# Optimization experiments

Measured on AMD Instinct MI355X. Metric: run time of the kernel, lower is better.

## Reference

```python
import jax, jax.numpy as jnp
import numpy as np
import math

D = 128
LAMBDA_INIT = 0.8 - 0.6 * math.exp(-0.3 * 1)  # depth=1


def _clin(xr, xi, wr, wi, br, bi):
    # complex linear: (xr + i xi) @ (wr + i wi)^T + (br + i bi)
    o_r = jnp.einsum('bhsd,od->bhso', xr, wr) - jnp.einsum('bhsd,od->bhso', xi, wi) + br
    o_i = jnp.einsum('bhsd,od->bhso', xr, wi) + jnp.einsum('bhsd,od->bhso', xi, wr) + bi
    return o_r, o_i


def setup_inputs() -> dict:
    key = jax.random.key(0)
    ks = jax.random.split(key, 32)
    B, H, S = 1, 12, 1024
    shp = (B, H, S, D)
    inp = {}
    names = ['q_r', 'q_i', 'k_r', 'k_i', 'v_r', 'v_i', 'pe_q_r', 'pe_q_i', 'pe_k_r', 'pe_k_i']
    for i, n in enumerate(names):
        inp[n] = jax.random.normal(ks[i], shp, dtype=jnp.float32)
    std = 1.0 / math.sqrt(D)
    inp['qw_r'] = jax.random.normal(ks[10], (2 * D, D), jnp.float32) * std
    inp['qw_i'] = jax.random.normal(ks[11], (2 * D, D), jnp.float32) * std
    inp['qb_r'] = jnp.zeros((2 * D,), jnp.float32)
    inp['qb_i'] = jnp.zeros((2 * D,), jnp.float32)
    for j, p in enumerate(['k', 'v', 'g', 'o']):
        inp[p + 'w_r'] = jax.random.normal(ks[12 + 2 * j], (D, D), jnp.float32) * std
        inp[p + 'w_i'] = jax.random.normal(ks[13 + 2 * j], (D, D), jnp.float32) * std
        inp[p + 'b_r'] = jnp.zeros((D,), jnp.float32)
        inp[p + 'b_i'] = jnp.zeros((D,), jnp.float32)
    inp['lq1'] = jax.random.normal(ks[20], (D,), jnp.float32) * 0.1
    inp['lk1'] = jax.random.normal(ks[21], (D,), jnp.float32) * 0.1
    inp['lq2'] = jax.random.normal(ks[22], (D,), jnp.float32) * 0.1
    inp['lk2'] = jax.random.normal(ks[23], (D,), jnp.float32) * 0.1
    inp['sub_w'] = jnp.ones((2 * D,), jnp.float32)
    return inp


def _forward(q_r, q_i, k_r, k_i, v_r, v_i, pe_q_r, pe_q_i, pe_k_r, pe_k_i,
             qw_r, qw_i, qb_r, qb_i, kw_r, kw_i, kb_r, kb_i,
             vw_r, vw_i, vb_r, vb_i, gw_r, gw_i, gb_r, gb_i,
             ow_r, ow_i, ob_r, ob_i, lq1, lk1, lq2, lk2, sub_w):
    scale = D ** (-0.5)
    qp_r, qp_i = _clin(q_r, q_i, qw_r, qw_i, qb_r, qb_i)   # [B,H,S,2D]
    kp_r, kp_i = _clin(k_r, k_i, kw_r, kw_i, kb_r, kb_i)   # [B,H,S,D]
    vp_r, vp_i = _clin(v_r, v_i, vw_r, vw_i, vb_r, vb_i)
    qp_r = qp_r + jnp.concatenate([pe_q_r, pe_q_r], axis=-1)
    qp_i = qp_i + jnp.concatenate([pe_q_i, pe_q_i], axis=-1)
    kp_r = kp_r + pe_k_r
    kp_i = kp_i + pe_k_i
    q1_r, q2_r = jnp.split(qp_r, 2, axis=-1)
    q1_i, q2_i = jnp.split(qp_i, 2, axis=-1)

    def attn_w(qr, qi):
        s_r = jnp.einsum('bhqd,bhkd->bhqk', qr, kp_r) + jnp.einsum('bhqd,bhkd->bhqk', qi, kp_i)
        s_i = jnp.einsum('bhqd,bhkd->bhqk', qi, kp_r) - jnp.einsum('bhqd,bhkd->bhqk', qr, kp_i)
        mag = jnp.sqrt(s_r ** 2 + s_i ** 2 + 1e-8) * scale
        return jax.nn.softmax(mag.astype(jnp.float32), axis=-1).astype(s_r.dtype)

    w1 = attn_w(q1_r, q1_i)
    w2 = attn_w(q2_r, q2_i)
    a1_r = jnp.einsum('bhqk,bhkd->bhqd', w1, vp_r)
    a1_i = jnp.einsum('bhqk,bhkd->bhqd', w1, vp_i)
    a2_r = jnp.einsum('bhqk,bhkd->bhqd', w2, vp_r)
    a2_i = jnp.einsum('bhqk,bhkd->bhqd', w2, vp_i)
    cat_r = jnp.concatenate([a1_r, a2_r], axis=-1)
    cat_i = jnp.concatenate([a1_i, a2_i], axis=-1)
    rms = jnp.sqrt(jnp.mean(cat_r ** 2 + cat_i ** 2, axis=-1, keepdims=True) + 1e-5)
    cat_r = cat_r / rms * sub_w
    cat_i = cat_i / rms * sub_w
    a1_r, a2_r = jnp.split(cat_r, 2, axis=-1)
    a1_i, a2_i = jnp.split(cat_i, 2, axis=-1)
    lam1 = jnp.exp(jnp.sum(lq1 * lk1))
    lam2 = jnp.exp(jnp.sum(lq2 * lk2))
    lam = jax.nn.sigmoid(lam1 - lam2 + LAMBDA_INIT)
    out_r = a1_r - lam * a2_r
    out_i = a1_i - lam * a2_i
    g_r, g_i = _clin(q_r, q_i, gw_r, gw_i, gb_r, gb_i)
    out_r, out_i = g_r * out_r - g_i * out_i, g_r * out_i + g_i * out_r
    out_r, out_i = _clin(out_r, out_i, ow_r, ow_i, ob_r, ob_i)
    return out_r, out_i


def reference(q_r, q_i, k_r, k_i, v_r, v_i, pe_q_r, pe_q_i, pe_k_r, pe_k_i,
              qw_r, qw_i, qb_r, qb_i, kw_r, kw_i, kb_r, kb_i,
              vw_r, vw_i, vb_r, vb_i, gw_r, gw_i, gb_r, gb_i,
              ow_r, ow_i, ob_r, ob_i, lq1, lk1, lq2, lk2, sub_w):
    return _forward(q_r, q_i, k_r, k_i, v_r, v_i, pe_q_r, pe_q_i, pe_k_r, pe_k_i,
                    qw_r, qw_i, qb_r, qb_i, kw_r, kw_i, kb_r, kb_i,
                    vw_r, vw_i, vb_r, vb_i, gw_r, gw_i, gb_r, gb_i,
                    ow_r, ow_i, ob_r, ob_i, lq1, lk1, lq2, lk2, sub_w)
```

## Files before the change

### kernel.cpp

```cpp
#include <hip/hip_runtime.h>
#include <math.h>

#define H 12
#define S 1024
#define D 128
#define NROWS (H * S)

typedef __attribute__((ext_vector_type(8))) _Float16 f16x8;
typedef __attribute__((ext_vector_type(4))) float f32x4;
typedef __attribute__((ext_vector_type(4))) int i32x4;

__device__ __forceinline__ short f2h(float f) {
    _Float16 h = (_Float16)f;
    return __builtin_bit_cast(short, h);
}
__device__ __forceinline__ float h2f(short s) {
    return (float)__builtin_bit_cast(_Float16, s);
}
__device__ __forceinline__ f16x8 fneg8(f16x8 v) {
    i32x4 u = __builtin_bit_cast(i32x4, v);
    u ^= (int)0x80008000;
    return __builtin_bit_cast(f16x8, u);
}

#define WS_QP_R   0ULL
#define WS_QP_I   6291456ULL
#define WS_KP_R   12582912ULL
#define WS_KP_I   15728640ULL
#define WS_VPT_R  18874368ULL
#define WS_VPT_I  22020096ULL
#define WS_GP_R   25165824ULL
#define WS_GP_I   28311552ULL
#define WS_ACAT_R 31457280ULL
#define WS_ACAT_I 37748736ULL
#define WS_LAM    44040192ULL
#define WS_SC     44040448ULL
#define W16_PER_HEAD   4194304ULL
#define STAT_PER_HEAD  16384ULL

__global__ void lam_kernel(const float* __restrict__ lq1, const float* __restrict__ lk1,
                           const float* __restrict__ lq2, const float* __restrict__ lk2,
                           float* __restrict__ lam_out)
{
    int t = threadIdx.x;
    float p1 = lq1[t] * lk1[t];
    float p2 = lq2[t] * lk2[t];
    #pragma unroll
    for (int off = 32; off; off >>= 1) {
        p1 += __shfl_xor(p1, off);
        p2 += __shfl_xor(p2, off);
    }
    __shared__ float s1[2], s2[2];
    if ((t & 63) == 0) { s1[t >> 6] = p1; s2[t >> 6] = p2; }
    __syncthreads();
    if (t == 0) {
        float l1 = expf(s1[0] + s1[1]);
        float l2 = expf(s2[0] + s2[1]);
        float x = l1 - l2 + 0.3555090675909693f;
        lam_out[0] = 1.0f / (1.0f + expf(-x));
    }
}

__global__ __launch_bounds__(256) void proj_all(
    const float* __restrict__ q_r, const float* __restrict__ q_i,
    const float* __restrict__ k_r, const float* __restrict__ k_i,
    const float* __restrict__ v_r, const float* __restrict__ v_i,
    const float* __restrict__ pe_q_r, const float* __restrict__ pe_q_i,
    const float* __restrict__ pe_k_r, const float* __restrict__ pe_k_i,
    const float* __restrict__ qw_r, const float* __restrict__ qw_i,
    const float* __restrict__ qb_r, const float* __restrict__ qb_i,
    const float* __restrict__ kw_r, const float* __restrict__ kw_i,
    const float* __restrict__ kb_r, const float* __restrict__ kb_i,
    const float* __restrict__ vw_r, const float* __restrict__ vw_i,
    const float* __restrict__ vb_r, const float* __restrict__ vb_i,
    const float* __restrict__ gw_r, const float* __restrict__ gw_i,
    const float* __restrict__ gb_r, const float* __restrict__ gb_i,
    short* __restrict__ qp_r, short* __restrict__ qp_i,
    short* __restrict__ kp_r, short* __restrict__ kp_i,
    short* __restrict__ vpT_r, short* __restrict__ vpT_i,
    short* __restrict__ gp_r, short* __restrict__ gp_i)
{
    const int y = blockIdx.y;
    const float *xr, *xi, *wr, *wi, *br, *bi, *per = nullptr, *pei = nullptr;
    short *outr_, *outi_;
    int M, omode, col0;
    if (y < 4)      { xr = q_r; xi = q_i; wr = qw_r; wi = qw_i; br = qb_r; bi = qb_i;
                      per = pe_q_r; pei = pe_q_i; outr_ = qp_r; outi_ = qp_i;
                      M = 256; omode = 1; col0 = y * 64; }
    else if (y < 6) { xr = k_r; xi = k_i; wr = kw_r; wi = kw_i; br = kb_r; bi = kb_i;
                      per = pe_k_r; pei = pe_k_i; outr_ = kp_r; outi_ = kp_i;
                      M = 128; omode = 1; col0 = (y - 4) * 64; }
    else if (y < 8) { xr = v_r; xi = v_i; wr = vw_r; wi = vw_i; br = vb_r; bi = vb_i;
                      outr_ = vpT_r; outi_ = vpT_i;
                      M = 128; omode = 2; col0 = (y - 6) * 64; }
    else            { xr = q_r; xi = q_i; wr = gw_r; wi = gw_i; br = gb_r; bi = gb_i;
                      outr_ = gp_r; outi_ = gp_i;
                      M = 128; omode = 1; col0 = (y - 8) * 64; }

    __shared__ short As[64 * 72], Brs[64 * 72], Bis[64 * 72];
    const int t = threadIdx.x;
    const int row0 = blockIdx.x * 64;
    const int lane = t & 63, wid = t >> 6;
    const int wm = (wid >> 1) * 32, wn = (wid & 1) * 32;
    const int fm = lane & 15, fq = lane >> 4;
    f32x4 zero4 = {0.f, 0.f, 0.f, 0.f};
    f32x4 accr[2][2], acci[2][2];
    #pragma unroll
    for (int i = 0; i < 2; ++i)
        #pragma unroll
        for (int j = 0; j < 2; ++j) { accr[i][j] = zero4; acci[i][j] = zero4; }

    for (int c = 0; c < 4; ++c) {
        const bool hi = (c >= 2);
        const int kb = (c & 1) * 64;
        const float* Asrc = hi ? xi : xr;
        const float* Brsrc = hi ? wi : wr;
        const float* Bisrc = hi ? wr : wi;
        const float bsign = hi ? -1.0f : 1.0f;
        __syncthreads();
        #pragma unroll
        for (int it = 0; it < 4; ++it) {
            int lin = it * 256 + t;
            int r = lin >> 4, k4 = (lin & 15) * 4;
            float4 va = *(const float4*)&Asrc[(size_t)(row0 + r) * 128 + kb + k4];
            *(short4*)&As[r * 72 + k4] = make_short4(f2h(va.x), f2h(va.y), f2h(va.z), f2h(va.w));
            float4 vr = *(const float4*)&Brsrc[(size_t)(col0 + r) * 128 + kb + k4];
            *(short4*)&Brs[r * 72 + k4] = make_short4(f2h(bsign * vr.x), f2h(bsign * vr.y),
                                                      f2h(bsign * vr.z), f2h(bsign * vr.w));
            float4 vi = *(const float4*)&Bisrc[(size_t)(col0 + r) * 128 + kb + k4];
            *(short4*)&Bis[r * 72 + k4] = make_short4(f2h(vi.x), f2h(vi.y), f2h(vi.z), f2h(vi.w));
        }
        __syncthreads();
        #pragma unroll
        for (int ks = 0; ks < 64; ks += 32) {
            f16x8 bfr[2], bfi[2];
            #pragma unroll
            for (int j = 0; j < 2; ++j) {
                bfr[j] = *(const f16x8*)&Brs[(wn + j * 16 + fm) * 72 + ks + fq * 8];
                bfi[j] = *(const f16x8*)&Bis[(wn + j * 16 + fm) * 72 + ks + fq * 8];
            }
            #pragma unroll
            for (int i = 0; i < 2; ++i) {
                f16x8 a = *(const f16x8*)&As[(wm + i * 16 + fm) * 72 + ks + fq * 8];
                #pragma unroll
                for (int j = 0; j < 2; ++j) {
                    accr[i][j] = __builtin_amdgcn_mfma_f32_16x16x32_f16(a, bfr[j], accr[i][j], 0, 0, 0);
                    acci[i][j] = __builtin_amdgcn_mfma_f32_16x16x32_f16(a, bfi[j], acci[i][j], 0, 0, 0);
                }
            }
        }
    }
    #pragma unroll
    for (int i = 0; i < 2; ++i)
        #pragma unroll
        for (int j = 0; j < 2; ++j) {
            int colc = col0 + wn + j * 16 + fm;
            float bbr = br[colc], bbi = bi[colc];
            if (omode == 2) {
                int rb = row0 + wm + i * 16 + fq * 4;
                int hq = rb >> 10, sq = rb & 1023;
                short4 o_r4 = make_short4(f2h(accr[i][j][0] + bbr), f2h(accr[i][j][1] + bbr),
                                          f2h(accr[i][j][2] + bbr), f2h(accr[i][j][3] + bbr));
                short4 o_i4 = make_short4(f2h(acci[i][j][0] + bbi), f2h(acci[i][j][1] + bbi),
                                          f2h(acci[i][j][2] + bbi), f2h(acci[i][j][3] + bbi));
                size_t ob = ((size_t)(hq * 128 + colc)) * 1024 + sq;
                *(short4*)&outr_[ob] = o_r4;
                *(short4*)&outi_[ob] = o_i4;
            } else {
                #pragma unroll
                for (int reg = 0; reg < 4; ++reg) {
                    int rr = row0 + wm + i * 16 + fq * 4 + reg;
                    float o_r = accr[i][j][reg] + bbr;
                    float o_i = acci[i][j][reg] + bbi;
                    if (per) {
                        o_r += per[(size_t)rr * 128 + (colc & 127)];
                        o_i += pei[(size_t)rr * 128 + (colc & 127)];
                    }
                    outr_[(size_t)rr * M + colc] = f2h(o_r);
                    outi_[(size_t)rr * M + colc] = f2h(o_i);
                }
            }
        }
}

__global__ __launch_bounds__(256) void oproj_mfma(
    const short* __restrict__ gp_r, const short* __restrict__ gp_i,
    const float* __restrict__ wr, const float* __restrict__ wi,
    const float* __restrict__ br, const float* __restrict__ bi,
    float* __restrict__ outr, float* __restrict__ outi)
{
    __shared__ short As[64 * 72], Brs[64 * 72], Bis[64 * 72];
    const int t = threadIdx.x;
    const int row0 = blockIdx.x * 64, col0 = blockIdx.y * 64;
    const int lane = t & 63, wid = t >> 6;
    const int wm = (wid >> 1) * 32, wn = (wid & 1) * 32;
    const int fm = lane & 15, fq = lane >> 4;
    f32x4 zero4 = {0.f, 0.f, 0.f, 0.f};
    f32x4 accr[2][2], acci[2][2];
    #pragma unroll
    for (int i = 0; i < 2; ++i)
        #pragma unroll
        for (int j = 0; j < 2; ++j) { accr[i][j] = zero4; acci[i][j] = zero4; }

    for (int c = 0; c < 4; ++c) {
        const bool hi = (c >= 2);
        const int kb = (c & 1) * 64;
        const short* Asrc = hi ? gp_i : gp_r;
        const float* Brsrc = hi ? wi : wr;
        const float* Bisrc = hi ? wr : wi;
        const float bsign = hi ? -1.0f : 1.0f;
        __syncthreads();
        #pragma unroll
        for (int it = 0; it < 4; ++it) {
            int lin = it * 256 + t;
            int r = lin >> 4, k4 = (lin & 15) * 4;
            *(short4*)&As[r * 72 + k4] = *(const short4*)&Asrc[(size_t)(row0 + r) * 128 + kb + k4];
            float4 vr = *(const float4*)&Brsrc[(size_t)(col0 + r) * 128 + kb + k4];
            *(short4*)&Brs[r * 72 + k4] = make_short4(f2h(bsign * vr.x), f2h(bsign * vr.y),
                                                      f2h(bsign * vr.z), f2h(bsign * vr.w));
            float4 vi = *(const float4*)&Bisrc[(size_t)(col0 + r) * 128 + kb + k4];
            *(short4*)&Bis[r * 72 + k4] = make_short4(f2h(vi.x), f2h(vi.y), f2h(vi.z), f2h(vi.w));
        }
        __syncthreads();
        #pragma unroll
        for (int ks = 0; ks < 64; ks += 32) {
            f16x8 bfr[2], bfi[2];
            #pragma unroll
            for (int j = 0; j < 2; ++j) {
                bfr[j] = *(const f16x8*)&Brs[(wn + j * 16 + fm) * 72 + ks + fq * 8];
                bfi[j] = *(const f16x8*)&Bis[(wn + j * 16 + fm) * 72 + ks + fq * 8];
            }
            #pragma unroll
            for (int i = 0; i < 2; ++i) {
                f16x8 a = *(const f16x8*)&As[(wm + i * 16 + fm) * 72 + ks + fq * 8];
                #pragma unroll
                for (int j = 0; j < 2; ++j) {
                    accr[i][j] = __builtin_amdgcn_mfma_f32_16x16x32_f16(a, bfr[j], accr[i][j], 0, 0, 0);
                    acci[i][j] = __builtin_amdgcn_mfma_f32_16x16x32_f16(a, bfi[j], acci[i][j], 0, 0, 0);
                }
            }
        }
    }
    #pragma unroll
    for (int i = 0; i < 2; ++i)
        #pragma unroll
        for (int j = 0; j < 2; ++j) {
            int colc = col0 + wn + j * 16 + fm;
            float bbr = br[colc], bbi = bi[colc];
            #pragma unroll
            for (int reg = 0; reg < 4; ++reg) {
                int rr = row0 + wm + i * 16 + fq * 4 + reg;
                outr[(size_t)rr * 128 + colc] = accr[i][j][reg] + bbr;
                outi[(size_t)rr * 128 + colc] = acci[i][j][reg] + bbi;
            }
        }
}

__global__ __launch_bounds__(256) void score_mfma(
    const short* __restrict__ qp_r, const short* __restrict__ qp_i,
    const short* __restrict__ kp_r, const short* __restrict__ kp_i,
    short* __restrict__ w16, int h0)
{
    __shared__ short Qr[64 * 72], Qi[64 * 72], Kt[128 * 72];
    const int t = threadIdx.x;
    const int hh = blockIdx.z >> 1, map = blockIdx.z & 1;
    const int h = h0 + hh;
    const int q0 = blockIdx.x * 64, c0 = blockIdx.y * 128;
    const int lane = t & 63, wid = t >> 6;
    const int wm = (wid >> 1) * 32, wn = (wid & 1) * 64;
    const int fm = lane & 15, fq = lane >> 4;
    f32x4 zero4 = {0.f, 0.f, 0.f, 0.f};
    f32x4 sr[2][4], si[2][4];
    #pragma unroll
    for (int i = 0; i < 2; ++i)
        #pragma unroll
        for (int j = 0; j < 4; ++j) { sr[i][j] = zero4; si[i][j] = zero4; }

    for (int kb = 0; kb < 2; ++kb) {
        const int kbase = map * 128 + kb * 64;
        __syncthreads();
        #pragma unroll
        for (int i = 0; i < 4; ++i) {
            int lin = i * 256 + t;
            int r = lin >> 4, k4 = (lin & 15) * 4;
            size_t qb = (size_t)(h * S + q0 + r) * 256 + kbase + k4;
            *(short4*)&Qr[r * 72 + k4] = *(const short4*)&qp_r[qb];
            *(short4*)&Qi[r * 72 + k4] = *(const short4*)&qp_i[qb];
        }
        #pragma unroll
        for (int i = 0; i < 8; ++i) {
            int lin = i * 256 + t;
            int r = lin >> 4, k4 = (lin & 15) * 4;
            *(short4*)&Kt[r * 72 + k4] =
                *(const short4*)&kp_r[(size_t)(h * S + c0 + r) * 128 + kb * 64 + k4];
        }
        __syncthreads();
        f16x8 aR[2][2], aI[2][2];
        #pragma unroll
        for (int ks = 0; ks < 2; ++ks)
            #pragma unroll
            for (int i = 0; i < 2; ++i) {
                int ao = (wm + i * 16 + fm) * 72 + ks * 32 + fq * 8;
                aR[ks][i] = *(const f16x8*)&Qr[ao];
                aI[ks][i] = *(const f16x8*)&Qi[ao];
            }
        #pragma unroll
        for (int ks = 0; ks < 2; ++ks) {
            f16x8 b[4];
            #pragma unroll
            for (int j = 0; j < 4; ++j)
                b[j] = *(const f16x8*)&Kt[(wn + j * 16 + fm) * 72 + ks * 32 + fq * 8];
            #pragma unroll
            for (int i = 0; i < 2; ++i)
                #pragma unroll
                for (int j = 0; j < 4; ++j) {
                    sr[i][j] = __builtin_amdgcn_mfma_f32_16x16x32_f16(aR[ks][i], b[j], sr[i][j], 0, 0, 0);
                    si[i][j] = __builtin_amdgcn_mfma_f32_16x16x32_f16(aI[ks][i], b[j], si[i][j], 0, 0, 0);
                }
        }
        __syncthreads();
        #pragma unroll
        for (int i = 0; i < 8; ++i) {
            int lin = i * 256 + t;
            int r = lin >> 4, k4 = (lin & 15) * 4;
            *(short4*)&Kt[r * 72 + k4] =
                *(const short4*)&kp_i[(size_t)(h * S + c0 + r) * 128 + kb * 64 + k4];
        }
        __syncthreads();
        #pragma unroll
        for (int ks = 0; ks < 2; ++ks) {
            f16x8 b[4];
            #pragma unroll
            for (int j = 0; j < 4; ++j)
                b[j] = *(const f16x8*)&Kt[(wn + j * 16 + fm) * 72 + ks * 32 + fq * 8];
            f16x8 nR0 = fneg8(aR[ks][0]), nR1 = fneg8(aR[ks][1]);
            #pragma unroll
            for (int j = 0; j < 4; ++j) {
                sr[0][j] = __builtin_amdgcn_mfma_f32_16x16x32_f16(aI[ks][0], b[j], sr[0][j], 0, 0, 0);
                si[0][j] = __builtin_amdgcn_mfma_f32_16x16x32_f16(nR0, b[j], si[0][j], 0, 0, 0);
                sr[1][j] = __builtin_amdgcn_mfma_f32_16x16x32_f16(aI[ks][1], b[j], sr[1][j], 0, 0, 0);
                si[1][j] = __builtin_amdgcn_mfma_f32_16x16x32_f16(nR1, b[j], si[1][j], 0, 0, 0);
            }
        }
    }
    const float scale = 0.08838834764831845f;
    #pragma unroll
    for (int i = 0; i < 2; ++i)
        #pragma unroll
        for (int j = 0; j < 4; ++j) {
            int kcol = c0 + wn + j * 16 + fm;
            #pragma unroll
            for (int reg = 0; reg < 4; ++reg) {
                int q = q0 + wm + i * 16 + fq * 4 + reg;
                float r1 = sr[i][j][reg], I1 = si[i][j][reg];
                float m1 = sqrtf(fmaf(r1, r1, fmaf(I1, I1, 1e-8f))) * scale;
                w16[(((size_t)hh * 2 + map) * S + q) * S + kcol] = f2h(m1);
            }
        }
}

__global__ __launch_bounds__(256) void smstats(const short* __restrict__ w16,
                                               float2* __restrict__ stats)
{
    const short* row = w16 + (size_t)blockIdx.x * S;
    int t = threadIdx.x;
    short4 s = ((const short4*)row)[t];
    float f0 = h2f(s.x), f1 = h2f(s.y), f2v = h2f(s.z), f3 = h2f(s.w);
    float m = fmaxf(fmaxf(f0, f1), fmaxf(f2v, f3));
    #pragma unroll
    for (int off = 32; off; off >>= 1) m = fmaxf(m, __shfl_xor(m, off));
    __shared__ float redm[4], reds[4];
    int w = t >> 6;
    if ((t & 63) == 0) redm[w] = m;
    __syncthreads();
    m = fmaxf(fmaxf(redm[0], redm[1]), fmaxf(redm[2], redm[3]));
    float ssum = __expf(f0 - m) + __expf(f1 - m) + __expf(f2v - m) + __expf(f3 - m);
    #pragma unroll
    for (int off = 32; off; off >>= 1) ssum += __shfl_xor(ssum, off);
    if ((t & 63) == 0) reds[w] = ssum;
    __syncthreads();
    if (t == 0) {
        float total = reds[0] + reds[1] + reds[2] + reds[3];
        stats[blockIdx.x] = make_float2(m, 1.0f / total);
    }
}

__global__ __launch_bounds__(256) void av_mfma(
    const short* __restrict__ w16, const float2* __restrict__ stats,
    const short* __restrict__ vpT_r, const short* __restrict__ vpT_i,
    short* __restrict__ acat_r, short* __restrict__ acat_i, int h0)
{
    __shared__ short W1[32 * 72], W2[32 * 72], Vc[128 * 72];
    const int t = threadIdx.x;
    const int hh = blockIdx.z, h = h0 + hh;
    const int comp = blockIdx.y;
    const int q0 = blockIdx.x * 32;
    const short* vpT = comp ? vpT_i : vpT_r;
    short* acat = comp ? acat_i : acat_r;
    const float2* st1 = stats + ((size_t)hh * 2 + 0) * S;
    const float2* st2 = stats + ((size_t)hh * 2 + 1) * S;
    const int lane = t & 63, wid = t >> 6;
    const int wm = (wid >> 1) * 16, wn = (wid & 1) * 64;
    const int fm = lane & 15, fq = lane >> 4;
    f32x4 zero4 = {0.f, 0.f, 0.f, 0.f};
    f32x4 a1[4], a2[4];
    #pragma unroll
    for (int j = 0; j < 4; ++j) { a1[j] = zero4; a2[j] = zero4; }

    for (int k0 = 0; k0 < S; k0 += 64) {
        __syncthreads();
        #pragma unroll
        for (int it = 0; it < 2; ++it) {
            int lin = it * 256 + t;
            int r = lin >> 4, k4 = (lin & 15) * 4;
            float2 s1v = st1[q0 + r];
            float2 s2v = st2[q0 + r];
            short4 m1 = *(const short4*)&w16[(((size_t)hh * 2 + 0) * S + q0 + r) * S + k0 + k4];
            short4 m2 = *(const short4*)&w16[(((size_t)hh * 2 + 1) * S + q0 + r) * S + k0 + k4];
            *(short4*)&W1[r * 72 + k4] = make_short4(
                f2h(__expf(h2f(m1.x) - s1v.x) * s1v.y), f2h(__expf(h2f(m1.y) - s1v.x) * s1v.y),
                f2h(__expf(h2f(m1.z) - s1v.x) * s1v.y), f2h(__expf(h2f(m1.w) - s1v.x) * s1v.y));
            *(short4*)&W2[r * 72 + k4] = make_short4(
                f2h(__expf(h2f(m2.x) - s2v.x) * s2v.y), f2h(__expf(h2f(m2.y) - s2v.x) * s2v.y),
                f2h(__expf(h2f(m2.z) - s2v.x) * s2v.y), f2h(__expf(h2f(m2.w) - s2v.x) * s2v.y));
        }
        #pragma unroll
        for (int it = 0; it < 8; ++it) {
            int lin = it * 256 + t;
            int dd = lin >> 4, k4 = (lin & 15) * 4;
            *(short4*)&Vc[dd * 72 + k4] = *(const short4*)&vpT[(size_t)(h * 128 + dd) * 1024 + k0 + k4];
        }
        __syncthreads();
        #pragma unroll
        for (int ks = 0; ks < 64; ks += 32) {
            f16x8 b[4];
            #pragma unroll
            for (int j = 0; j < 4; ++j)
                b[j] = *(const f16x8*)&Vc[(wn + j * 16 + fm) * 72 + ks + fq * 8];
            int wo = (wm + fm) * 72 + ks + fq * 8;
            f16x8 w1f = *(const f16x8*)&W1[wo];
            f16x8 w2f = *(const f16x8*)&W2[wo];
            #pragma unroll
            for (int j = 0; j < 4; ++j) {
                a1[j] = __builtin_amdgcn_mfma_f32_16x16x32_f16(w1f, b[j], a1[j], 0, 0, 0);
                a2[j] = __builtin_amdgcn_mfma_f32_16x16x32_f16(w2f, b[j], a2[j], 0, 0, 0);
            }
        }
    }
    #pragma unroll
    for (int j = 0; j < 4; ++j) {
        int d = wn + j * 16 + fm;
        #pragma unroll
        for (int reg = 0; reg < 4; ++reg) {
            int q = q0 + wm + fq * 4 + reg;
            size_t rowb = (size_t)(h * S + q) * 256;
            acat[rowb + d]       = f2h(a1[j][reg]);
            acat[rowb + 128 + d] = f2h(a2[j][reg]);
        }
    }
}

__global__ __launch_bounds__(256) void rmsgate_kernel(
    const short* __restrict__ acat_r, const short* __restrict__ acat_i,
    const float* __restrict__ sub_w, const float* __restrict__ lam_ptr,
    short* __restrict__ gp_r, short* __restrict__ gp_i)
{
    int row = blockIdx.x;
    int t = threadIdx.x;
    float ar = h2f(acat_r[(size_t)row * 256 + t]);
    float ai = h2f(acat_i[(size_t)row * 256 + t]);
    float ss = fmaf(ar, ar, ai * ai);
    #pragma unroll
    for (int off = 32; off; off >>= 1) ss += __shfl_xor(ss, off);
    __shared__ float red[4];
    if ((t & 63) == 0) red[t >> 6] = ss;
    __syncthreads();
    float total = red[0] + red[1] + red[2] + red[3];
    float inv_rms = 1.0f / sqrtf(total * (1.0f / 256.0f) + 1e-5f);
    float sw = sub_w[t];
    __shared__ float Cr[256], Ci[256];
    Cr[t] = ar * inv_rms * sw;
    Ci[t] = ai * inv_rms * sw;
    __syncthreads();
    if (t < 128) {
        float lam = lam_ptr[0];
        float o_r = Cr[t] - lam * Cr[t + 128];
        float o_i = Ci[t] - lam * Ci[t + 128];
        float gr = h2f(gp_r[(size_t)row * 128 + t]);
        float gi = h2f(gp_i[(size_t)row * 128 + t]);
        gp_r[(size_t)row * 128 + t] = f2h(gr * o_r - gi * o_i);
        gp_i[(size_t)row * 128 + t] = f2h(gr * o_i + gi * o_r);
    }
}

extern "C" void kernel_launch(void* const* d_in, const int* in_sizes, int n_in,
                              void* d_out, int out_size, void* d_ws, size_t ws_size,
                              hipStream_t stream)
{
    (void)in_sizes; (void)n_in; (void)out_size;
    const float* q_r    = (const float*)d_in[0];
    const float* q_i    = (const float*)d_in[1];
    const float* k_r    = (const float*)d_in[2];
    const float* k_i    = (const float*)d_in[3];
    const float* v_r    = (const float*)d_in[4];
    const float* v_i    = (const float*)d_in[5];
    const float* pe_q_r = (const float*)d_in[6];
    const float* pe_q_i = (const float*)d_in[7];
    const float* pe_k_r = (const float*)d_in[8];
    const float* pe_k_i = (const float*)d_in[9];
    const float* qw_r   = (const float*)d_in[10];
    const float* qw_i   = (const float*)d_in[11];
    const float* qb_r   = (const float*)d_in[12];
    const float* qb_i   = (const float*)d_in[13];
    const float* kw_r   = (const float*)d_in[14];
    const float* kw_i   = (const float*)d_in[15];
    const float* kb_r   = (const float*)d_in[16];
    const float* kb_i   = (const float*)d_in[17];
    const float* vw_r   = (const float*)d_in[18];
    const float* vw_i   = (const float*)d_in[19];
    const float* vb_r   = (const float*)d_in[20];
    const float* vb_i   = (const float*)d_in[21];
    const float* gw_r   = (const float*)d_in[22];
    const float* gw_i   = (const float*)d_in[23];
    const float* gb_r   = (const float*)d_in[24];
    const float* gb_i   = (const float*)d_in[25];
    const float* ow_r   = (const float*)d_in[26];
    const float* ow_i   = (const float*)d_in[27];
    const float* ob_r   = (const float*)d_in[28];
    const float* ob_i   = (const float*)d_in[29];
    const float* lq1    = (const float*)d_in[30];
    const float* lk1    = (const float*)d_in[31];
    const float* lq2    = (const float*)d_in[32];
    const float* lk2    = (const float*)d_in[33];
    const float* sub_w  = (const float*)d_in[34];

    char* ws = (char*)d_ws;
    short* qp_r   = (short*)(ws + WS_QP_R);
    short* qp_i   = (short*)(ws + WS_QP_I);
    short* kp_r   = (short*)(ws + WS_KP_R);
    short* kp_i   = (short*)(ws + WS_KP_I);
    short* vpT_r  = (short*)(ws + WS_VPT_R);
    short* vpT_i  = (short*)(ws + WS_VPT_I);
    short* gp_r   = (short*)(ws + WS_GP_R);
    short* gp_i   = (short*)(ws + WS_GP_I);
    short* acat_r = (short*)(ws + WS_ACAT_R);
    short* acat_i = (short*)(ws + WS_ACAT_I);
    float* lam    = (float*)(ws + WS_LAM);
    short* w16    = (short*)(ws + WS_SC);

    float* out_r = (float*)d_out;
    float* out_i = out_r + (size_t)NROWS * D;

    size_t avail = ws_size > WS_SC ? ws_size - WS_SC : 0;
    int nh_chunk = (int)(avail / (W16_PER_HEAD + STAT_PER_HEAD));
    if (nh_chunk < 1) nh_chunk = 1;
    if (nh_chunk > H) nh_chunk = H;
    float2* stats = (float2*)(ws + WS_SC + (size_t)nh_chunk * W16_PER_HEAD);

    lam_kernel<<<1, 128, 0, stream>>>(lq1, lk1, lq2, lk2, lam);

    proj_all<<<dim3(192, 10), 256, 0, stream>>>(
        q_r, q_i, k_r, k_i, v_r, v_i, pe_q_r, pe_q_i, pe_k_r, pe_k_i,
        qw_r, qw_i, qb_r, qb_i, kw_r, kw_i, kb_r, kb_i,
        vw_r, vw_i, vb_r, vb_i, gw_r, gw_i, gb_r, gb_i,
        qp_r, qp_i, kp_r, kp_i, vpT_r, vpT_i, gp_r, gp_i);

    for (int h0 = 0; h0 < H; h0 += nh_chunk) {
        int nhh = (H - h0 < nh_chunk) ? (H - h0) : nh_chunk;
        score_mfma<<<dim3(16, 8, nhh * 2), 256, 0, stream>>>(qp_r, qp_i, kp_r, kp_i, w16, h0);
        smstats<<<nhh * 2 * S, 256, 0, stream>>>(w16, stats);
        av_mfma<<<dim3(32, 2, nhh), 256, 0, stream>>>(w16, stats, vpT_r, vpT_i, acat_r, acat_i, h0);
    }

    rmsgate_kernel<<<NROWS, 256, 0, stream>>>(acat_r, acat_i, sub_w, lam, gp_r, gp_i);

    oproj_mfma<<<dim3(192, 2), 256, 0, stream>>>(gp_r, gp_i, ow_r, ow_i, ob_r, ob_i, out_r, out_i);
}
```

Measured before the change: 296.7 us.

## Fuse all stages into one cooperative persistent kernel with grid syncs

Turns projection, score, softmax stats, AV, RMS-gate and output projection into device functions run by a single persistent cooperative kernel, with grid-wide barriers between stages, and keeps the multi-launch path as a fallback. The aim is to remove the per-launch overhead and tail idle time of about seven separate kernel launches. In exchange, grid.sync barriers add their own cost and work is spread over a fixed grid (up to 2048 blocks), so per-stage load balance and occupancy may get worse. The cooperative path only runs when the workspace is large enough to hold all heads at once.

```diff
diff --git a/kernel.cpp b/kernel.cpp
--- a/kernel.cpp
+++ b/kernel.cpp
@@ -1,5 +1,8 @@
 #include <hip/hip_runtime.h>
+#include <hip/hip_cooperative_groups.h>
 #include <math.h>
+
+namespace cg = cooperative_groups;
 
 #define H 12
 #define S 1024
@@ -37,69 +40,47 @@
 #define WS_SC     44040448ULL
 #define W16_PER_HEAD   4194304ULL
 #define STAT_PER_HEAD  16384ULL
-
-__global__ void lam_kernel(const float* __restrict__ lq1, const float* __restrict__ lk1,
-                           const float* __restrict__ lq2, const float* __restrict__ lk2,
-                           float* __restrict__ lam_out)
-{
-    int t = threadIdx.x;
-    float p1 = lq1[t] * lk1[t];
-    float p2 = lq2[t] * lk2[t];
-    #pragma unroll
-    for (int off = 32; off; off >>= 1) {
-        p1 += __shfl_xor(p1, off);
-        p2 += __shfl_xor(p2, off);
-    }
-    __shared__ float s1[2], s2[2];
-    if ((t & 63) == 0) { s1[t >> 6] = p1; s2[t >> 6] = p2; }
-    __syncthreads();
-    if (t == 0) {
-        float l1 = expf(s1[0] + s1[1]);
-        float l2 = expf(s2[0] + s2[1]);
-        float x = l1 - l2 + 0.3555090675909693f;
-        lam_out[0] = 1.0f / (1.0f + expf(-x));
-    }
-}
-
-__global__ __launch_bounds__(256) void proj_all(
-    const float* __restrict__ q_r, const float* __restrict__ q_i,
-    const float* __restrict__ k_r, const float* __restrict__ k_i,
-    const float* __restrict__ v_r, const float* __restrict__ v_i,
-    const float* __restrict__ pe_q_r, const float* __restrict__ pe_q_i,
-    const float* __restrict__ pe_k_r, const float* __restrict__ pe_k_i,
-    const float* __restrict__ qw_r, const float* __restrict__ qw_i,
-    const float* __restrict__ qb_r, const float* __restrict__ qb_i,
-    const float* __restrict__ kw_r, const float* __restrict__ kw_i,
-    const float* __restrict__ kb_r, const float* __restrict__ kb_i,
-    const float* __restrict__ vw_r, const float* __restrict__ vw_i,
-    const float* __restrict__ vb_r, const float* __restrict__ vb_i,
-    const float* __restrict__ gw_r, const float* __restrict__ gw_i,
-    const float* __restrict__ gb_r, const float* __restrict__ gb_i,
-    short* __restrict__ qp_r, short* __restrict__ qp_i,
-    short* __restrict__ kp_r, short* __restrict__ kp_i,
-    short* __restrict__ vpT_r, short* __restrict__ vpT_i,
-    short* __restrict__ gp_r, short* __restrict__ gp_i)
-{
-    const int y = blockIdx.y;
+#define WS_STATS_FULL  (WS_SC + 12ULL * W16_PER_HEAD)
+#define WS_NEED_FULL   (WS_STATS_FULL + 24576ULL * 8ULL)
+
+struct MegaParams {
+    const float *q_r, *q_i, *k_r, *k_i, *v_r, *v_i;
+    const float *pe_q_r, *pe_q_i, *pe_k_r, *pe_k_i;
+    const float *qw_r, *qw_i, *qb_r, *qb_i;
+    const float *kw_r, *kw_i, *kb_r, *kb_i;
+    const float *vw_r, *vw_i, *vb_r, *vb_i;
+    const float *gw_r, *gw_i, *gb_r, *gb_i;
+    const float *ow_r, *ow_i, *ob_r, *ob_i;
+    const float *lq1, *lk1, *lq2, *lk2, *sub_w;
+    short *qp_r, *qp_i, *kp_r, *kp_i, *vpT_r, *vpT_i, *gp_r, *gp_i;
+    short *acat_r, *acat_i;
+    short *w16;
+    float *lam;
+    float2 *stats;
+    float *out_r, *out_i;
+};
+
+__device__ __forceinline__ void dev_proj(int bxx, int y, short* As, short* Brs, short* Bis,
+                                         const MegaParams& P)
+{
     const float *xr, *xi, *wr, *wi, *br, *bi, *per = nullptr, *pei = nullptr;
     short *outr_, *outi_;
     int M, omode, col0;
-    if (y < 4)      { xr = q_r; xi = q_i; wr = qw_r; wi = qw_i; br = qb_r; bi = qb_i;
-                      per = pe_q_r; pei = pe_q_i; outr_ = qp_r; outi_ = qp_i;
+    if (y < 4)      { xr = P.q_r; xi = P.q_i; wr = P.qw_r; wi = P.qw_i; br = P.qb_r; bi = P.qb_i;
+                      per = P.pe_q_r; pei = P.pe_q_i; outr_ = P.qp_r; outi_ = P.qp_i;
                       M = 256; omode = 1; col0 = y * 64; }
-    else if (y < 6) { xr = k_r; xi = k_i; wr = kw_r; wi = kw_i; br = kb_r; bi = kb_i;
-                      per = pe_k_r; pei = pe_k_i; outr_ = kp_r; outi_ = kp_i;
+    else if (y < 6) { xr = P.k_r; xi = P.k_i; wr = P.kw_r; wi = P.kw_i; br = P.kb_r; bi = P.kb_i;
+                      per = P.pe_k_r; pei = P.pe_k_i; outr_ = P.kp_r; outi_ = P.kp_i;
                       M = 128; omode = 1; col0 = (y - 4) * 64; }
-    else if (y < 8) { xr = v_r; xi = v_i; wr = vw_r; wi = vw_i; br = vb_r; bi = vb_i;
-                      outr_ = vpT_r; outi_ = vpT_i;
+    else if (y < 8) { xr = P.v_r; xi = P.v_i; wr = P.vw_r; wi = P.vw_i; br = P.vb_r; bi = P.vb_i;
+                      outr_ = P.vpT_r; outi_ = P.vpT_i;
                       M = 128; omode = 2; col0 = (y - 6) * 64; }
-    else            { xr = q_r; xi = q_i; wr = gw_r; wi = gw_i; br = gb_r; bi = gb_i;
-                      outr_ = gp_r; outi_ = gp_i;
+    else            { xr = P.q_r; xi = P.q_i; wr = P.gw_r; wi = P.gw_i; br = P.gb_r; bi = P.gb_i;
+                      outr_ = P.gp_r; outi_ = P.gp_i;
                       M = 128; omode = 1; col0 = (y - 8) * 64; }
 
-    __shared__ short As[64 * 72], Brs[64 * 72], Bis[64 * 72];
     const int t = threadIdx.x;
-    const int row0 = blockIdx.x * 64;
+    const int row0 = bxx * 64;
     const int lane = t & 63, wid = t >> 6;
     const int wm = (wid >> 1) * 32, wn = (wid & 1) * 32;
     const int fm = lane & 15, fq = lane >> 4;
@@ -183,15 +164,182 @@
         }
 }
 
-__global__ __launch_bounds__(256) void oproj_mfma(
-    const short* __restrict__ gp_r, const short* __restrict__ gp_i,
-    const float* __restrict__ wr, const float* __restrict__ wi,
-    const float* __restrict__ br, const float* __restrict__ bi,
-    float* __restrict__ outr, float* __restrict__ outi)
-{
-    __shared__ short As[64 * 72], Brs[64 * 72], Bis[64 * 72];
+__device__ __forceinline__ void dev_score(int bxx, int byy, int hhL, int map, int h,
+                                          short* Qr, short* Qi, short* Kt,
+                                          const MegaParams& P, short* w16)
+{
     const int t = threadIdx.x;
-    const int row0 = blockIdx.x * 64, col0 = blockIdx.y * 64;
+    const int q0 = bxx * 64, c0 = byy * 128;
+    const int lane = t & 63, wid = t >> 6;
+    const int wm = (wid >> 1) * 32, wn = (wid & 1) * 64;
+    const int fm = lane & 15, fq = lane >> 4;
+    f32x4 zero4 = {0.f, 0.f, 0.f, 0.f};
+    f32x4 sr[2][4], si[2][4];
+    #pragma unroll
+    for (int i = 0; i < 2; ++i)
+        #pragma unroll
+        for (int j = 0; j < 4; ++j) { sr[i][j] = zero4; si[i][j] = zero4; }
+
+    for (int kb = 0; kb < 2; ++kb) {
+        const int kbase = map * 128 + kb * 64;
+        __syncthreads();
+        #pragma unroll
+        for (int i = 0; i < 4; ++i) {
+            int lin = i * 256 + t;
+            int r = lin >> 4, k4 = (lin & 15) * 4;
+            size_t qb = (size_t)(h * S + q0 + r) * 256 + kbase + k4;
+            *(short4*)&Qr[r * 72 + k4] = *(const short4*)&P.qp_r[qb];
+            *(short4*)&Qi[r * 72 + k4] = *(const short4*)&P.qp_i[qb];
+        }
+        #pragma unroll
+        for (int i = 0; i < 8; ++i) {
+            int lin = i * 256 + t;
+            int r = lin >> 4, k4 = (lin & 15) * 4;
+            *(short4*)&Kt[r * 72 + k4] =
+                *(const short4*)&P.kp_r[(size_t)(h * S + c0 + r) * 128 + kb * 64 + k4];
+        }
+        __syncthreads();
+        f16x8 aR[2][2], aI[2][2];
+        #pragma unroll
+        for (int ks = 0; ks < 2; ++ks)
+            #pragma unroll
+            for (int i = 0; i < 2; ++i) {
+                int ao = (wm + i * 16 + fm) * 72 + ks * 32 + fq * 8;
+                aR[ks][i] = *(const f16x8*)&Qr[ao];
+                aI[ks][i] = *(const f16x8*)&Qi[ao];
+            }
+        #pragma unroll
+        for (int ks = 0; ks < 2; ++ks) {
+            f16x8 b[4];
+            #pragma unroll
+            for (int j = 0; j < 4; ++j)
+                b[j] = *(const f16x8*)&Kt[(wn + j * 16 + fm) * 72 + ks * 32 + fq * 8];
+            #pragma unroll
+            for (int i = 0; i < 2; ++i)
+                #pragma unroll
+                for (int j = 0; j < 4; ++j) {
+                    sr[i][j] = __builtin_amdgcn_mfma_f32_16x16x32_f16(aR[ks][i], b[j], sr[i][j], 0, 0, 0);
+                    si[i][j] = __builtin_amdgcn_mfma_f32_16x16x32_f16(aI[ks][i], b[j], si[i][j], 0, 0, 0);
+                }
+        }
+        __syncthreads();
+        #pragma unroll
+        for (int i = 0; i < 8; ++i) {
+            int lin = i * 256 + t;
+            int r = lin >> 4, k4 = (lin & 15) * 4;
+            *(short4*)&Kt[r * 72 + k4] =
+                *(const short4*)&P.kp_i[(size_t)(h * S + c0 + r) * 128 + kb * 64 + k4];
+        }
+        __syncthreads();
+        #pragma unroll
+        for (int ks = 0; ks < 2; ++ks) {
+            f16x8 b[4];
+            #pragma unroll
+            for (int j = 0; j < 4; ++j)
+                b[j] = *(const f16x8*)&Kt[(wn + j * 16 + fm) * 72 + ks * 32 + fq * 8];
+            f16x8 nR0 = fneg8(aR[ks][0]), nR1 = fneg8(aR[ks][1]);
+            #pragma unroll
+            for (int j = 0; j < 4; ++j) {
+                sr[0][j] = __builtin_amdgcn_mfma_f32_16x16x32_f16(aI[ks][0], b[j], sr[0][j], 0, 0, 0);
+                si[0][j] = __builtin_amdgcn_mfma_f32_16x16x32_f16(nR0, b[j], si[0][j], 0, 0, 0);
+                sr[1][j] = __builtin_amdgcn_mfma_f32_16x16x32_f16(aI[ks][1], b[j], sr[1][j], 0, 0, 0);
+                si[1][j] = __builtin_amdgcn_mfma_f32_16x16x32_f16(nR1, b[j], si[1][j], 0, 0, 0);
+            }
+        }
+    }
+    const float scale = 0.08838834764831845f;
+    #pragma unroll
+    for (int i = 0; i < 2; ++i)
+        #pragma unroll
+        for (int j = 0; j < 4; ++j) {
+            int kcol = c0 + wn + j * 16 + fm;
+            #pragma unroll
+            for (int reg = 0; reg < 4; ++reg) {
+                int q = q0 + wm + i * 16 + fq * 4 + reg;
+                float r1 = sr[i][j][reg], I1 = si[i][j][reg];
+                float m1 = sqrtf(fmaf(r1, r1, fmaf(I1, I1, 1e-8f))) * scale;
+                w16[(((size_t)hhL * 2 + map) * S + q) * S + kcol] = f2h(m1);
+            }
+        }
+}
+
+__device__ __forceinline__ void dev_av(int bxx, int comp, int hhL, int h,
+                                       short* W1, short* W2, short* Vc,
+                                       const MegaParams& P, const short* w16,
+                                       const float2* stats)
+{
+    const int t = threadIdx.x;
+    const int q0 = bxx * 32;
+    const short* vpT = comp ? P.vpT_i : P.vpT_r;
+    short* acat = comp ? P.acat_i : P.acat_r;
+    const float2* st1 = stats + ((size_t)hhL * 2 + 0) * S;
+    const float2* st2 = stats + ((size_t)hhL * 2 + 1) * S;
+    const int lane = t & 63, wid = t >> 6;
+    const int wm = (wid >> 1) * 16, wn = (wid & 1) * 64;
+    const int fm = lane & 15, fq = lane >> 4;
+    f32x4 zero4 = {0.f, 0.f, 0.f, 0.f};
+    f32x4 a1[4], a2[4];
+    #pragma unroll
+    for (int j = 0; j < 4; ++j) { a1[j] = zero4; a2[j] = zero4; }
+
+    for (int k0 = 0; k0 < S; k0 += 64) {
+        __syncthreads();
+        #pragma unroll
+        for (int it = 0; it < 2; ++it) {
+            int lin = it * 256 + t;
+            int r = lin >> 4, k4 = (lin & 15) * 4;
+            float2 s1v = st1[q0 + r];
+            float2 s2v = st2[q0 + r];
+            short4 m1 = *(const short4*)&w16[(((size_t)hhL * 2 + 0) * S + q0 + r) * S + k0 + k4];
+            short4 m2 = *(const short4*)&w16[(((size_t)hhL * 2 + 1) * S + q0 + r) * S + k0 + k4];
+            *(short4*)&W1[r * 72 + k4] = make_short4(
+                f2h(__expf(h2f(m1.x) - s1v.x) * s1v.y), f2h(__expf(h2f(m1.y) - s1v.x) * s1v.y),
+                f2h(__expf(h2f(m1.z) - s1v.x) * s1v.y), f2h(__expf(h2f(m1.w) - s1v.x) * s1v.y));
+            *(short4*)&W2[r * 72 + k4] = make_short4(
+                f2h(__expf(h2f(m2.x) - s2v.x) * s2v.y), f2h(__expf(h2f(m2.y) - s2v.x) * s2v.y),
+                f2h(__expf(h2f(m2.z) - s2v.x) * s2v.y), f2h(__expf(h2f(m2.w) - s2v.x) * s2v.y));
+        }
+        #pragma unroll
+        for (int it = 0; it < 8; ++it) {
+            int lin = it * 256 + t;
+            int dd = lin >> 4, k4 = (lin & 15) * 4;
+            *(short4*)&Vc[dd * 72 + k4] = *(const short4*)&vpT[(size_t)(h * 128 + dd) * 1024 + k0 + k4];
+        }
+        __syncthreads();
+        #pragma unroll
+        for (int ks = 0; ks < 64; ks += 32) {
+            f16x8 b[4];
+            #pragma unroll
+            for (int j = 0; j < 4; ++j)
+                b[j] = *(const f16x8*)&Vc[(wn + j * 16 + fm) * 72 + ks + fq * 8];
+            int wo = (wm + fm) * 72 + ks + fq * 8;
+            f16x8 w1f = *(const f16x8*)&W1[wo];
+            f16x8 w2f = *(const f16x8*)&W2[wo];
+            #pragma unroll
+            for (int j = 0; j < 4; ++j) {
+                a1[j] = __builtin_amdgcn_mfma_f32_16x16x32_f16(w1f, b[j], a1[j], 0, 0, 0);
+                a2[j] = __builtin_amdgcn_mfma_f32_16x16x32_f16(w2f, b[j], a2[j], 0, 0, 0);
+            }
+        }
+    }
+    #pragma unroll
+    for (int j = 0; j < 4; ++j) {
+        int d = wn + j * 16 + fm;
+        #pragma unroll
+        for (int reg = 0; reg < 4; ++reg) {
+            int q = q0 + wm + fq * 4 + reg;
+            size_t rowb = (size_t)(h * S + q) * 256;
+            acat[rowb + d]       = f2h(a1[j][reg]);
+            acat[rowb + 128 + d] = f2h(a2[j][reg]);
+        }
+    }
+}
+
+__device__ __forceinline__ void dev_oproj(int bxx, int byy, short* As, short* Brs, short* Bis,
+                                          const MegaParams& P)
+{
+    const int t = threadIdx.x;
+    const int row0 = bxx * 64, col0 = byy * 64;
     const int lane = t & 63, wid = t >> 6;
     const int wm = (wid >> 1) * 32, wn = (wid & 1) * 32;
     const int fm = lane & 15, fq = lane >> 4;
@@ -205,9 +353,9 @@
     for (int c = 0; c < 4; ++c) {
         const bool hi = (c >= 2);
         const int kb = (c & 1) * 64;
-        const short* Asrc = hi ? gp_i : gp_r;
-        const float* Brsrc = hi ? wi : wr;
-        const float* Bisrc = hi ? wr : wi;
+        const short* Asrc = hi ? P.gp_i : P.gp_r;
+        const float* Brsrc = hi ? P.ow_i : P.ow_r;
+        const float* Bisrc = hi ? P.ow_r : P.ow_i;
         const float bsign = hi ? -1.0f : 1.0f;
         __syncthreads();
         #pragma unroll
@@ -246,123 +394,188 @@
         #pragma unroll
         for (int j = 0; j < 2; ++j) {
             int colc = col0 + wn + j * 16 + fm;
-            float bbr = br[colc], bbi = bi[colc];
+            float bbr = P.ob_r[colc], bbi = P.ob_i[colc];
             #pragma unroll
             for (int reg = 0; reg < 4; ++reg) {
                 int rr = row0 + wm + i * 16 + fq * 4 + reg;
-                outr[(size_t)rr * 128 + colc] = accr[i][j][reg] + bbr;
-                outi[(size_t)rr * 128 + colc] = acci[i][j][reg] + bbi;
-            }
-        }
-}
-
-__global__ __launch_bounds__(256) void score_mfma(
-    const short* __restrict__ qp_r, const short* __restrict__ qp_i,
-    const short* __restrict__ kp_r, const short* __restrict__ kp_i,
-    short* __restrict__ w16, int h0)
-{
-    __shared__ short Qr[64 * 72], Qi[64 * 72], Kt[128 * 72];
-    const int t = threadIdx.x;
-    const int hh = blockIdx.z >> 1, map = blockIdx.z & 1;
-    const int h = h0 + hh;
-    const int q0 = blockIdx.x * 64, c0 = blockIdx.y * 128;
-    const int lane = t & 63, wid = t >> 6;
-    const int wm = (wid >> 1) * 32, wn = (wid & 1) * 64;
-    const int fm = lane & 15, fq = lane >> 4;
-    f32x4 zero4 = {0.f, 0.f, 0.f, 0.f};
-    f32x4 sr[2][4], si[2][4];
-    #pragma unroll
-    for (int i = 0; i < 2; ++i)
-        #pragma unroll
-        for (int j = 0; j < 4; ++j) { sr[i][j] = zero4; si[i][j] = zero4; }
-
-    for (int kb = 0; kb < 2; ++kb) {
-        const int kbase = map * 128 + kb * 64;
-        __syncthreads();
-        #pragma unroll
-        for (int i = 0; i < 4; ++i) {
-            int lin = i * 256 + t;
-            int r = lin >> 4, k4 = (lin & 15) * 4;
-            size_t qb = (size_t)(h * S + q0 + r) * 256 + kbase + k4;
-            *(short4*)&Qr[r * 72 + k4] = *(const short4*)&qp_r[qb];
-            *(short4*)&Qi[r * 72 + k4] = *(const short4*)&qp_i[qb];
-        }
-        #pragma unroll
-        for (int i = 0; i < 8; ++i) {
-            int lin = i * 256 + t;
-            int r = lin >> 4, k4 = (lin & 15) * 4;
-            *(short4*)&Kt[r * 72 + k4] =
-                *(const short4*)&kp_r[(size_t)(h * S + c0 + r) * 128 + kb * 64 + k4];
-        }
-        __syncthreads();
-        f16x8 aR[2][2], aI[2][2];
-        #pragma unroll
-        for (int ks = 0; ks < 2; ++ks)
-            #pragma unroll
-            for (int i = 0; i < 2; ++i) {
-                int ao = (wm + i * 16 + fm) * 72 + ks * 32 + fq * 8;
-                aR[ks][i] = *(const f16x8*)&Qr[ao];
-                aI[ks][i] = *(const f16x8*)&Qi[ao];
-            }
-        #pragma unroll
-        for (int ks = 0; ks < 2; ++ks) {
-            f16x8 b[4];
-            #pragma unroll
-            for (int j = 0; j < 4; ++j)
-                b[j] = *(const f16x8*)&Kt[(wn + j * 16 + fm) * 72 + ks * 32 + fq * 8];
-            #pragma unroll
-            for (int i = 0; i < 2; ++i)
+                P.out_r[(size_t)rr * 128 + colc] = accr[i][j][reg] + bbr;
+                P.out_i[(size_t)rr * 128 + colc] = acci[i][j][reg] + bbi;
+            }
+        }
+}
+
+__global__ __launch_bounds__(256) void mega(MegaParams P)
+{
+    cg::grid_group gg = cg::this_grid();
+    __shared__ __align__(16) char SM[36864];
+    const int nb = (int)gridDim.x, bid = (int)blockIdx.x;
+    const int t = threadIdx.x, lane = t & 63, wid = t >> 6;
+
+    {
+        float p1 = (t < 128) ? P.lq1[t] * P.lk1[t] : 0.f;
+        float p2 = (t < 128) ? P.lq2[t] * P.lk2[t] : 0.f;
+        #pragma unroll
+        for (int off = 32; off; off >>= 1) {
+            p1 += __shfl_xor(p1, off);
+            p2 += __shfl_xor(p2, off);
+        }
+        float* s1 = (float*)SM;
+        float* s2 = s1 + 4;
+        if ((t & 63) == 0) { s1[wid] = p1; s2[wid] = p2; }
+        __syncthreads();
+        if (bid == 0 && t == 0) {
+            float l1 = expf(s1[0] + s1[1] + s1[2] + s1[3]);
+            float l2 = expf(s2[0] + s2[1] + s2[2] + s2[3]);
+            float x = l1 - l2 + 0.3555090675909693f;
+            P.lam[0] = 1.0f / (1.0f + expf(-x));
+        }
+        __syncthreads();
+    }
+
+    {
+        short* As = (short*)SM;
+        short* Brs = As + 64 * 72;
+        short* Bis = Brs + 64 * 72;
+        for (int it = bid; it < 1920; it += nb)
+            dev_proj(it % 192, it / 192, As, Brs, Bis, P);
+    }
+    gg.sync();
+
+    {
+        short* Qr = (short*)SM;
+        short* Qi = Qr + 64 * 72;
+        short* Kt = Qi + 64 * 72;
+        for (int it = bid; it < 3072; it += nb) {
+            int z = it / 128;
+            dev_score(it % 16, (it / 16) % 8, z >> 1, z & 1, z >> 1, Qr, Qi, Kt, P, P.w16);
+        }
+    }
+    gg.sync();
+
+    for (int row = bid * 4 + wid; row < 2 * NROWS; row += nb * 4) {
+        const short* rp = P.w16 + (size_t)row * S;
+        short4 v0 = ((const short4*)rp)[lane];
+        short4 v1 = ((const short4*)rp)[lane + 64];
+        short4 v2 = ((const short4*)rp)[lane + 128];
+        short4 v3 = ((const short4*)rp)[lane + 192];
+        float f[16] = {h2f(v0.x), h2f(v0.y), h2f(v0.z), h2f(v0.w),
+                       h2f(v1.x), h2f(v1.y), h2f(v1.z), h2f(v1.w),
+                       h2f(v2.x), h2f(v2.y), h2f(v2.z), h2f(v2.w),
+                       h2f(v3.x), h2f(v3.y), h2f(v3.z), h2f(v3.w)};
+        float m = f[0];
+        #pragma unroll
+        for (int j = 1; j < 16; ++j) m = fmaxf(m, f[j]);
+        #pragma unroll
+        for (int off = 32; off; off >>= 1) m = fmaxf(m, __shfl_xor(m, off));
+        float ssum = 0.f;
+        #pragma unroll
+        for (int j = 0; j < 16; ++j) ssum += __expf(f[j] - m);
+        #pragma unroll
+        for (int off = 32; off; off >>= 1) ssum += __shfl_xor(ssum, off);
+        if (lane == 0) P.stats[row] = make_float2(m, 1.0f / ssum);
+    }
+    gg.sync();
+
+    {
+        short* W1 = (short*)SM;
+        short* W2 = W1 + 32 * 72;
+        short* Vc = W2 + 32 * 72;
+        for (int it = bid; it < 768; it += nb)
+            dev_av(it % 32, (it / 32) % 2, it / 64, it / 64, W1, W2, Vc, P, P.w16, P.stats);
+    }
+    gg.sync();
+
+    {
+        const float lam = P.lam[0];
+        for (int row = bid * 4 + wid; row < NROWS; row += nb * 4) {
+            short4 ar4 = ((const short4*)(P.acat_r + (size_t)row * 256))[lane];
+            short4 ai4 = ((const short4*)(P.acat_i + (size_t)row * 256))[lane];
+            float ar[4] = {h2f(ar4.x), h2f(ar4.y), h2f(ar4.z), h2f(ar4.w)};
+            float ai[4] = {h2f(ai4.x), h2f(ai4.y), h2f(ai4.z), h2f(ai4.w)};
+            float ss = 0.f;
+            #pragma unroll
+            for (int j = 0; j < 4; ++j) ss = fmaf(ar[j], ar[j], fmaf(ai[j], ai[j], ss));
+            #pragma unroll
+            for (int off = 32; off; off >>= 1) ss += __shfl_xor(ss, off);
+            float inv_rms = 1.0f / sqrtf(ss * (1.0f / 256.0f) + 1e-5f);
+            float4 sw = ((const float4*)P.sub_w)[lane];
+            float Cr[4], Ci[4];
+            Cr[0] = ar[0] * inv_rms * sw.x; Ci[0] = ai[0] * inv_rms * sw.x;
+            Cr[1] = ar[1] * inv_rms * sw.y; Ci[1] = ai[1] * inv_rms * sw.y;
+            Cr[2] = ar[2] * inv_rms * sw.z; Ci[2] = ai[2] * inv_rms * sw.z;
+            Cr[3] = ar[3] * inv_rms * sw.w; Ci[3] = ai[3] * inv_rms * sw.w;
+            float pr[4], pi[4];
+            #pragma unroll
+            for (int j = 0; j < 4; ++j) {
+                pr[j] = __shfl_xor(Cr[j], 32);
+                pi[j] = __shfl_xor(Ci[j], 32);
+            }
+            if (lane < 32) {
+                short4 gr4 = ((const short4*)(P.gp_r + (size_t)row * 128))[lane];
+                short4 gi4 = ((const short4*)(P.gp_i + (size_t)row * 128))[lane];
+                float grv[4] = {h2f(gr4.x), h2f(gr4.y), h2f(gr4.z), h2f(gr4.w)};
+                float giv[4] = {h2f(gi4.x), h2f(gi4.y), h2f(gi4.z), h2f(gi4.w)};
+                short orx[4], oix[4];
                 #pragma unroll
                 for (int j = 0; j < 4; ++j) {
-                    sr[i][j] = __builtin_amdgcn_mfma_f32_16x16x32_f16(aR[ks][i], b[j], sr[i][j], 0, 0, 0);
-                    si[i][j] = __builtin_amdgcn_mfma_f32_16x16x32_f16(aI[ks][i], b[j], si[i][j], 0, 0, 0);
+                    float o_r = Cr[j] - lam * pr[j];
+                    float o_i = Ci[j] - lam * pi[j];
+                    orx[j] = f2h(grv[j] * o_r - giv[j] * o_i);
+                    oix[j] = f2h(grv[j] * o_i + giv[j] * o_r);
                 }
-        }
-        __syncthreads();
-        #pragma unroll
-        for (int i = 0; i < 8; ++i) {
-            int lin = i * 256 + t;
-            int r = lin >> 4, k4 = (lin & 15) * 4;
-            *(short4*)&Kt[r * 72 + k4] =
-                *(const short4*)&kp_i[(size_t)(h * S + c0 + r) * 128 + kb * 64 + k4];
-        }
-        __syncthreads();
-        #pragma unroll
-        for (int ks = 0; ks < 2; ++ks) {
-            f16x8 b[4];
-            #pragma unroll
-            for (int j = 0; j < 4; ++j)
-                b[j] = *(const f16x8*)&Kt[(wn + j * 16 + fm) * 72 + ks * 32 + fq * 8];
-            f16x8 nR0 = fneg8(aR[ks][0]), nR1 = fneg8(aR[ks][1]);
-            #pragma unroll
-            for (int j = 0; j < 4; ++j) {
-                sr[0][j] = __builtin_amdgcn_mfma_f32_16x16x32_f16(aI[ks][0], b[j], sr[0][j], 0, 0, 0);
-                si[0][j] = __builtin_amdgcn_mfma_f32_16x16x32_f16(nR0, b[j], si[0][j], 0, 0, 0);
-                sr[1][j] = __builtin_amdgcn_mfma_f32_16x16x32_f16(aI[ks][1], b[j], sr[1][j], 0, 0, 0);
-                si[1][j] = __builtin_amdgcn_mfma_f32_16x16x32_f16(nR1, b[j], si[1][j], 0, 0, 0);
-            }
-        }
-    }
-    const float scale = 0.08838834764831845f;
-    #pragma unroll
-    for (int i = 0; i < 2; ++i)
-        #pragma unroll
-        for (int j = 0; j < 4; ++j) {
-            int kcol = c0 + wn + j * 16 + fm;
-            #pragma unroll
-            for (int reg = 0; reg < 4; ++reg) {
-                int q = q0 + wm + i * 16 + fq * 4 + reg;
-                float r1 = sr[i][j][reg], I1 = si[i][j][reg];
-                float m1 = sqrtf(fmaf(r1, r1, fmaf(I1, I1, 1e-8f))) * scale;
-                w16[(((size_t)hh * 2 + map) * S + q) * S + kcol] = f2h(m1);
-            }
-        }
-}
-
-__global__ __launch_bounds__(256) void smstats(const short* __restrict__ w16,
-                                               float2* __restrict__ stats)
-{
-    const short* row = w16 + (size_t)blockIdx.x * S;
+                ((short4*)(P.gp_r + (size_t)row * 128))[lane] = make_short4(orx[0], orx[1], orx[2], orx[3]);
+                ((short4*)(P.gp_i + (size_t)row * 128))[lane] = make_short4(oix[0], oix[1], oix[2], oix[3]);
+            }
+        }
+    }
+    gg.sync();
+
+    {
+        short* As = (short*)SM;
+        short* Brs = As + 64 * 72;
+        short* Bis = Brs + 64 * 72;
+        for (int it = bid; it < 384; it += nb)
+            dev_oproj(it % 192, it / 192, As, Brs, Bis, P);
+    }
+}
+
+__global__ void lam_k(MegaParams P)
+{
+    int t = threadIdx.x;
+    float p1 = P.lq1[t] * P.lk1[t];
+    float p2 = P.lq2[t] * P.lk2[t];
+    #pragma unroll
+    for (int off = 32; off; off >>= 1) {
+        p1 += __shfl_xor(p1, off);
+        p2 += __shfl_xor(p2, off);
+    }
+    __shared__ float s1[2], s2[2];
+    if ((t & 63) == 0) { s1[t >> 6] = p1; s2[t >> 6] = p2; }
+    __syncthreads();
+    if (t == 0) {
+        float l1 = expf(s1[0] + s1[1]);
+        float l2 = expf(s2[0] + s2[1]);
+        float x = l1 - l2 + 0.3555090675909693f;
+        P.lam[0] = 1.0f / (1.0f + expf(-x));
+    }
+}
+
+__global__ __launch_bounds__(256) void proj_k(MegaParams P)
+{
+    __shared__ short As[64 * 72], Brs[64 * 72], Bis[64 * 72];
+    dev_proj(blockIdx.x, blockIdx.y, As, Brs, Bis, P);
+}
+
+__global__ __launch_bounds__(256) void score_k(MegaParams P, int h0)
+{
+    __shared__ short Qr[64 * 72], Qi[64 * 72], Kt[128 * 72];
+    int z = blockIdx.z;
+    dev_score(blockIdx.x, blockIdx.y, z >> 1, z & 1, h0 + (z >> 1), Qr, Qi, Kt, P, P.w16);
+}
+
+__global__ __launch_bounds__(256) void smstats_k(MegaParams P, float2* stats)
+{
+    const short* row = P.w16 + (size_t)blockIdx.x * S;
     int t = threadIdx.x;
     short4 s = ((const short4*)row)[t];
     float f0 = h2f(s.x), f1 = h2f(s.y), f2v = h2f(s.z), f3 = h2f(s.w);
@@ -385,90 +598,18 @@
     }
 }
 
-__global__ __launch_bounds__(256) void av_mfma(
-    const short* __restrict__ w16, const float2* __restrict__ stats,
-    const short* __restrict__ vpT_r, const short* __restrict__ vpT_i,
-    short* __restrict__ acat_r, short* __restrict__ acat_i, int h0)
+__global__ __launch_bounds__(256) void av_k(MegaParams P, float2* stats, int h0)
 {
     __shared__ short W1[32 * 72], W2[32 * 72], Vc[128 * 72];
-    const int t = threadIdx.x;
-    const int hh = blockIdx.z, h = h0 + hh;
-    const int comp = blockIdx.y;
-    const int q0 = blockIdx.x * 32;
-    const short* vpT = comp ? vpT_i : vpT_r;
-    short* acat = comp ? acat_i : acat_r;
-    const float2* st1 = stats + ((size_t)hh * 2 + 0) * S;
-    const float2* st2 = stats + ((size_t)hh * 2 + 1) * S;
-    const int lane = t & 63, wid = t >> 6;
-    const int wm = (wid >> 1) * 16, wn = (wid & 1) * 64;
-    const int fm = lane & 15, fq = lane >> 4;
-    f32x4 zero4 = {0.f, 0.f, 0.f, 0.f};
-    f32x4 a1[4], a2[4];
-    #pragma unroll
-    for (int j = 0; j < 4; ++j) { a1[j] = zero4; a2[j] = zero4; }
-
-    for (int k0 = 0; k0 < S; k0 += 64) {
-        __syncthreads();
-        #pragma unroll
-        for (int it = 0; it < 2; ++it) {
-            int lin = it * 256 + t;
-            int r = lin >> 4, k4 = (lin & 15) * 4;
-            float2 s1v = st1[q0 + r];
-            float2 s2v = st2[q0 + r];
-            short4 m1 = *(const short4*)&w16[(((size_t)hh * 2 + 0) * S + q0 + r) * S + k0 + k4];
-            short4 m2 = *(const short4*)&w16[(((size_t)hh * 2 + 1) * S + q0 + r) * S + k0 + k4];
-            *(short4*)&W1[r * 72 + k4] = make_short4(
-                f2h(__expf(h2f(m1.x) - s1v.x) * s1v.y), f2h(__expf(h2f(m1.y) - s1v.x) * s1v.y),
-                f2h(__expf(h2f(m1.z) - s1v.x) * s1v.y), f2h(__expf(h2f(m1.w) - s1v.x) * s1v.y));
-            *(short4*)&W2[r * 72 + k4] = make_short4(
-                f2h(__expf(h2f(m2.x) - s2v.x) * s2v.y), f2h(__expf(h2f(m2.y) - s2v.x) * s2v.y),
-                f2h(__expf(h2f(m2.z) - s2v.x) * s2v.y), f2h(__expf(h2f(m2.w) - s2v.x) * s2v.y));
-        }
-        #pragma unroll
-        for (int it = 0; it < 8; ++it) {
-            int lin = it * 256 + t;
-            int dd = lin >> 4, k4 = (lin & 15) * 4;
-            *(short4*)&Vc[dd * 72 + k4] = *(const short4*)&vpT[(size_t)(h * 128 + dd) * 1024 + k0 + k4];
-        }
-        __syncthreads();
-        #pragma unroll
-        for (int ks = 0; ks < 64; ks += 32) {
-            f16x8 b[4];
-            #pragma unroll
-            for (int j = 0; j < 4; ++j)
-                b[j] = *(const f16x8*)&Vc[(wn + j * 16 + fm) * 72 + ks + fq * 8];
-            int wo = (wm + fm) * 72 + ks + fq * 8;
-            f16x8 w1f = *(const f16x8*)&W1[wo];
-            f16x8 w2f = *(const f16x8*)&W2[wo];
-            #pragma unroll
-            for (int j = 0; j < 4; ++j) {
-                a1[j] = __builtin_amdgcn_mfma_f32_16x16x32_f16(w1f, b[j], a1[j], 0, 0, 0);
-                a2[j] = __builtin_amdgcn_mfma_f32_16x16x32_f16(w2f, b[j], a2[j], 0, 0, 0);
-            }
-        }
-    }
-    #pragma unroll
-    for (int j = 0; j < 4; ++j) {
-        int d = wn + j * 16 + fm;
-        #pragma unroll
-        for (int reg = 0; reg < 4; ++reg) {
-            int q = q0 + wm + fq * 4 + reg;
-            size_t rowb = (size_t)(h * S + q) * 256;
-            acat[rowb + d]       = f2h(a1[j][reg]);
-            acat[rowb + 128 + d] = f2h(a2[j][reg]);
-        }
-    }
-}
-
-__global__ __launch_bounds__(256) void rmsgate_kernel(
-    const short* __restrict__ acat_r, const short* __restrict__ acat_i,
-    const float* __restrict__ sub_w, const float* __restrict__ lam_ptr,
-    short* __restrict__ gp_r, short* __restrict__ gp_i)
+    dev_av(blockIdx.x, blockIdx.y, blockIdx.z, h0 + blockIdx.z, W1, W2, Vc, P, P.w16, stats);
+}
+
+__global__ __launch_bounds__(256) void rmsgate_k(MegaParams P)
 {
     int row = blockIdx.x;
     int t = threadIdx.x;
-    float ar = h2f(acat_r[(size_t)row * 256 + t]);
-    float ai = h2f(acat_i[(size_t)row * 256 + t]);
+    float ar = h2f(P.acat_r[(size_t)row * 256 + t]);
+    float ai = h2f(P.acat_i[(size_t)row * 256 + t]);
     float ss = fmaf(ar, ar, ai * ai);
     #pragma unroll
     for (int off = 32; off; off >>= 1) ss += __shfl_xor(ss, off);
@@ -477,20 +618,26 @@
     __syncthreads();
     float total = red[0] + red[1] + red[2] + red[3];
     float inv_rms = 1.0f / sqrtf(total * (1.0f / 256.0f) + 1e-5f);
-    float sw = sub_w[t];
+    float sw = P.sub_w[t];
     __shared__ float Cr[256], Ci[256];
     Cr[t] = ar * inv_rms * sw;
     Ci[t] = ai * inv_rms * sw;
     __syncthreads();
     if (t < 128) {
-        float lam = lam_ptr[0];
+        float lam = P.lam[0];
         float o_r = Cr[t] - lam * Cr[t + 128];
         float o_i = Ci[t] - lam * Ci[t + 128];
-        float gr = h2f(gp_r[(size_t)row * 128 + t]);
-        float gi = h2f(gp_i[(size_t)row * 128 + t]);
-        gp_r[(size_t)row * 128 + t] = f2h(gr * o_r - gi * o_i);
-        gp_i[(size_t)row * 128 + t] = f2h(gr * o_i + gi * o_r);
-    }
+        float gr = h2f(P.gp_r[(size_t)row * 128 + t]);
+        float gi = h2f(P.gp_i[(size_t)row * 128 + t]);
+        P.gp_r[(size_t)row * 128 + t] = f2h(gr * o_r - gi * o_i);
+        P.gp_i[(size_t)row * 128 + t] = f2h(gr * o_i + gi * o_r);
+    }
+}
+
+__global__ __launch_bounds__(256) void oproj_k(MegaParams P)
+{
+    __shared__ short As[64 * 72], Brs[64 * 72], Bis[64 * 72];
+    dev_oproj(blockIdx.x, blockIdx.y, As, Brs, Bis, P);
 }
 
 extern "C" void kernel_launch(void* const* d_in, const int* in_sizes, int n_in,
@@ -498,58 +645,53 @@
                               hipStream_t stream)
 {
     (void)in_sizes; (void)n_in; (void)out_size;
-    const float* q_r    = (const float*)d_in[0];
-    const float* q_i    = (const float*)d_in[1];
-    const float* k_r    = (const float*)d_in[2];
-    const float* k_i    = (const float*)d_in[3];
-    const float* v_r    = (const float*)d_in[4];
-    const float* v_i    = (const float*)d_in[5];
-    const float* pe_q_r = (const float*)d_in[6];
-    const float* pe_q_i = (const float*)d_in[7];
-    const float* pe_k_r = (const float*)d_in[8];
-    const float* pe_k_i = (const float*)d_in[9];
-    const float* qw_r   = (const float*)d_in[10];
-    const float* qw_i   = (const float*)d_in[11];
-    const float* qb_r   = (const float*)d_in[12];
-    const float* qb_i   = (const float*)d_in[13];
-    const float* kw_r   = (const float*)d_in[14];
-    const float* kw_i   = (const float*)d_in[15];
-    const float* kb_r   = (const float*)d_in[16];
-    const float* kb_i   = (const float*)d_in[17];
-    const float* vw_r   = (const float*)d_in[18];
-    const float* vw_i   = (const float*)d_in[19];
-    const float* vb_r   = (const float*)d_in[20];
-    const float* vb_i   = (const float*)d_in[21];
-    const float* gw_r   = (const float*)d_in[22];
-    const float* gw_i   = (const float*)d_in[23];
-    const float* gb_r   = (const float*)d_in[24];
-    const float* gb_i   = (const float*)d_in[25];
-    const float* ow_r   = (const float*)d_in[26];
-    const float* ow_i   = (const float*)d_in[27];
-    const float* ob_r   = (const float*)d_in[28];
-    const float* ob_i   = (const float*)d_in[29];
-    const float* lq1    = (const float*)d_in[30];
-    const float* lk1    = (const float*)d_in[31];
-    const float* lq2    = (const float*)d_in[32];
-    const float* lk2    = (const float*)d_in[33];
-    const float* sub_w  = (const float*)d_in[34];
-
     char* ws = (char*)d_ws;
-    short* qp_r   = (short*)(ws + WS_QP_R);
-    short* qp_i   = (short*)(ws + WS_QP_I);
-    short* kp_r   = (short*)(ws + WS_KP_R);
-    short* kp_i   = (short*)(ws + WS_KP_I);
-    short* vpT_r  = (short*)(ws + WS_VPT_R);
-    short* vpT_i  = (short*)(ws + WS_VPT_I);
-    short* gp_r   = (short*)(ws + WS_GP_R);
-    short* gp_i   = (short*)(ws + WS_GP_I);
-    short* acat_r = (short*)(ws + WS_ACAT_R);
-    short* acat_i = (short*)(ws + WS_ACAT_I);
-    float* lam    = (float*)(ws + WS_LAM);
-    short* w16    = (short*)(ws + WS_SC);
-
-    float* out_r = (float*)d_out;
-    float* out_i = out_r + (size_t)NROWS * D;
+
+    MegaParams P;
+    P.q_r    = (const float*)d_in[0];  P.q_i    = (const float*)d_in[1];
+    P.k_r    = (const float*)d_in[2];  P.k_i    = (const float*)d_in[3];
+    P.v_r    = (const float*)d_in[4];  P.v_i    = (const float*)d_in[5];
+    P.pe_q_r = (const float*)d_in[6];  P.pe_q_i = (const float*)d_in[7];
+    P.pe_k_r = (const float*)d_in[8];  P.pe_k_i = (const float*)d_in[9];
+    P.qw_r   = (const float*)d_in[10]; P.qw_i   = (const float*)d_in[11];
+    P.qb_r   = (const float*)d_in[12]; P.qb_i   = (const float*)d_in[13];
+    P.kw_r   = (const float*)d_in[14]; P.kw_i   = (const float*)d_in[15];
+    P.kb_r   = (const float*)d_in[16]; P.kb_i   = (const float*)d_in[17];
+    P.vw_r   = (const float*)d_in[18]; P.vw_i   = (const float*)d_in[19];
+    P.vb_r   = (const float*)d_in[20]; P.vb_i   = (const float*)d_in[21];
+    P.gw_r   = (const float*)d_in[22]; P.gw_i   = (const float*)d_in[23];
+    P.gb_r   = (const float*)d_in[24]; P.gb_i   = (const float*)d_in[25];
+    P.ow_r   = (const float*)d_in[26]; P.ow_i   = (const float*)d_in[27];
+    P.ob_r   = (const float*)d_in[28]; P.ob_i   = (const float*)d_in[29];
+    P.lq1    = (const float*)d_in[30]; P.lk1    = (const float*)d_in[31];
+    P.lq2    = (const float*)d_in[32]; P.lk2    = (const float*)d_in[33];
+    P.sub_w  = (const float*)d_in[34];
+
+    P.qp_r   = (short*)(ws + WS_QP_R);   P.qp_i   = (short*)(ws + WS_QP_I);
+    P.kp_r   = (short*)(ws + WS_KP_R);   P.kp_i   = (short*)(ws + WS_KP_I);
+    P.vpT_r  = (short*)(ws + WS_VPT_R);  P.vpT_i  = (short*)(ws + WS_VPT_I);
+    P.gp_r   = (short*)(ws + WS_GP_R);   P.gp_i   = (short*)(ws + WS_GP_I);
+    P.acat_r = (short*)(ws + WS_ACAT_R); P.acat_i = (short*)(ws + WS_ACAT_I);
+    P.lam    = (float*)(ws + WS_LAM);
+    P.w16    = (short*)(ws + WS_SC);
+    P.stats  = (float2*)(ws + WS_STATS_FULL);
+    P.out_r  = (float*)d_out;
+    P.out_i  = P.out_r + (size_t)NROWS * D;
+
+    static int s_coopGrid = -2;
+    if (s_coopGrid == -2) {
+        int maxb = 0;
+        hipError_t e = hipOccupancyMaxActiveBlocksPerMultiprocessor(&maxb, mega, 256, 0);
+        s_coopGrid = (e == hipSuccess && maxb >= 1) ? maxb * 256  : 0;
+        if (s_coopGrid > 2048) s_coopGrid = 2048;
+    }
+    if (s_coopGrid > 0 && ws_size >= WS_NEED_FULL) {
+        void* args[] = {(void*)&P};
+        hipError_t e = hipLaunchCooperativeKernel(mega, dim3(s_coopGrid), dim3(256),
+                                                  args, 0, stream);
+        if (e == hipSuccess) return;
+        s_coopGrid = 0;
+    }
 
     size_t avail = ws_size > WS_SC ? ws_size - WS_SC : 0;
     int nh_chunk = (int)(avail / (W16_PER_HEAD + STAT_PER_HEAD));
@@ -557,22 +699,14 @@
     if (nh_chunk > H) nh_chunk = H;
     float2* stats = (float2*)(ws + WS_SC + (size_t)nh_chunk * W16_PER_HEAD);
 
-    lam_kernel<<<1, 128, 0, stream>>>(lq1, lk1, lq2, lk2, lam);
-
-    proj_all<<<dim3(192, 10), 256, 0, stream>>>(
-        q_r, q_i, k_r, k_i, v_r, v_i, pe_q_r, pe_q_i, pe_k_r, pe_k_i,
-        qw_r, qw_i, qb_r, qb_i, kw_r, kw_i, kb_r, kb_i,
-        vw_r, vw_i, vb_r, vb_i, gw_r, gw_i, gb_r, gb_i,
-        qp_r, qp_i, kp_r, kp_i, vpT_r, vpT_i, gp_r, gp_i);
-
+    lam_k<<<1, 128, 0, stream>>>(P);
+    proj_k<<<dim3(192, 10), 256, 0, stream>>>(P);
     for (int h0 = 0; h0 < H; h0 += nh_chunk) {
         int nhh = (H - h0 < nh_chunk) ? (H - h0) : nh_chunk;
-        score_mfma<<<dim3(16, 8, nhh * 2), 256, 0, stream>>>(qp_r, qp_i, kp_r, kp_i, w16, h0);
-        smstats<<<nhh * 2 * S, 256, 0, stream>>>(w16, stats);
-        av_mfma<<<dim3(32, 2, nhh), 256, 0, stream>>>(w16, stats, vpT_r, vpT_i, acat_r, acat_i, h0);
-    }
-
-    rmsgate_kernel<<<NROWS, 256, 0, stream>>>(acat_r, acat_i, sub_w, lam, gp_r, gp_i);
-
-    oproj_mfma<<<dim3(192, 2), 256, 0, stream>>>(gp_r, gp_i, ow_r, ow_i, ob_r, ob_i, out_r, out_i);
-}
+        score_k<<<dim3(16, 8, nhh * 2), 256, 0, stream>>>(P, h0);
+        smstats_k<<<nhh * 2 * S, 256, 0, stream>>>(P, stats);
+        av_k<<<dim3(32, 2, nhh), 256, 0, stream>>>(P, stats, h0);
+    }
+    rmsgate_k<<<NROWS, 256, 0, stream>>>(P);
+    oproj_k<<<dim3(192, 2), 256, 0, stream>>>(P);
+}
```

New measurement: 303.5 us. +2.3%, slower.
